# Performance work log

Measured on AMD Instinct MI355X. Metric: run time of the kernel, lower is better.

Reference implementation:

```python
import jax, jax.numpy as jnp
import numpy as np

EPS = 1e-5

def setup_inputs() -> dict:
    key = jax.random.key(0)
    ks = jax.random.split(key, 10)
    B, S, C, Q, D = 16, 2048, 768, 1024, 64
    clamp3_features = jax.random.normal(ks[0], (B, S, C), dtype=jnp.float32)
    residual = jax.random.normal(ks[1], (B, S, Q), dtype=jnp.float32)
    # params (xavier-ish scale; up-proj given small random values instead of zeros
    # so the output is non-trivial for correctness testing)
    Wproj = jax.random.normal(ks[2], (Q, C), dtype=jnp.float32) * (1.0 / np.sqrt(C))
    Wdown = jax.random.normal(ks[3], (D, Q), dtype=jnp.float32) * (1.0 / np.sqrt(Q))
    gamma = jnp.ones((D,), dtype=jnp.float32)
    beta = jnp.zeros((D,), dtype=jnp.float32)
    Wl1 = jax.random.normal(ks[4], (D, D), dtype=jnp.float32) * (1.0 / np.sqrt(D))
    bl1 = jnp.zeros((D,), dtype=jnp.float32)
    Wl2 = jax.random.normal(ks[5], (D, D), dtype=jnp.float32) * (1.0 / np.sqrt(D))
    bl2 = jnp.zeros((D,), dtype=jnp.float32)
    Wup = jax.random.normal(ks[6], (Q, D), dtype=jnp.float32) * (1.0 / np.sqrt(D))
    return {"clamp3_features": clamp3_features, "residual": residual,
            "Wproj": Wproj, "Wdown": Wdown, "gamma": gamma, "beta": beta,
            "Wl1": Wl1, "bl1": bl1, "Wl2": Wl2, "bl2": bl2, "Wup": Wup}

def _layernorm(x, gamma, beta):
    mu = jnp.mean(x, axis=-1, keepdims=True)
    var = jnp.mean(jnp.square(x - mu), axis=-1, keepdims=True)
    return (x - mu) * jax.lax.rsqrt(var + EPS) * gamma + beta

def reference(clamp3_features, residual, Wproj, Wdown, gamma, beta, Wl1, bl1, Wl2, bl2, Wup):
    # projection (no bias) -> down (no bias) -> LayerNorm
    projected = jnp.einsum('bsc,qc->bsq', clamp3_features, Wproj)
    down = jnp.einsum('bsq,dq->bsd', projected, Wdown)
    normed = _layernorm(down, gamma, beta)
    # SwiGLU: swish(l1(x)) * l2(x)
    o1 = jnp.einsum('bsd,ed->bse', normed, Wl1) + bl1
    swish = o1 * jax.nn.sigmoid(o1)
    gate = jnp.einsum('bsd,ed->bse', normed, Wl2) + bl2
    activated = swish * gate  # dropout is identity in eval mode
    up = jnp.einsum('bsd,qd->bsq', activated, Wup)
    return residual + up
```

## Files before the change

### kernel.cpp

```cpp
#include <hip/hip_runtime.h>


#define CDIM 768
#define QDIM 1024

typedef __attribute__((ext_vector_type(8))) short bf16x8;
typedef __attribute__((ext_vector_type(4))) float f32x4;

__device__ __forceinline__ ushort f2bf(float f) {
  union { float f; unsigned u; } v; v.f = f;
  unsigned r = v.u + 0x7fffu + ((v.u >> 16) & 1u);
  return (ushort)(r >> 16);
}

__device__ __forceinline__ void gload16(const float* g, float* lds) {
  __builtin_amdgcn_global_load_lds(
      (const __attribute__((address_space(1))) void*)g,
      (__attribute__((address_space(3))) void*)lds, 16, 0, 0);
}

__global__ void k_wcomb(const float* __restrict__ Wproj, const float* __restrict__ Wdown,
                        float* __restrict__ part) {
  int bid = blockIdx.x;
  int cb = bid % 12, db = (bid / 12) % 8, qc = bid / 96;
  int l = threadIdx.x;
  int c = cb * 64 + l;
  float acc[8];
  #pragma unroll
  for (int i = 0; i < 8; ++i) acc[i] = 0.f;
  int q0 = qc * 128;
  for (int q = q0; q < q0 + 128; ++q) {
    float xp = Wproj[q * CDIM + c];
    #pragma unroll
    for (int i = 0; i < 8; ++i)
      acc[i] = fmaf(Wdown[(db * 8 + i) * QDIM + q], xp, acc[i]);
  }
  #pragma unroll
  for (int i = 0; i < 8; ++i)
    part[((size_t)qc * CDIM + c) * 64 + db * 8 + i] = acc[i];
}

__global__ void k_arrange(const float* __restrict__ part, const float* __restrict__ Wup,
                          const float* __restrict__ Wl1, const float* __restrict__ Wl2,
                          ushort* __restrict__ wcf, ushort* __restrict__ wupf,
                          ushort* __restrict__ wl1f, ushort* __restrict__ wl2f) {
  int idx = blockIdx.x * 256 + threadIdx.x;
  if (idx < 49152) {
    int i0 = idx;
    int j = i0 & 7, l = (i0 >> 3) & 63, t = i0 >> 9;
    int g = l >> 4, r16 = l & 15;
    int nf = t & 3, ks = t >> 2;
    int k = 32 * ks + 8 * g + j, n = 16 * nf + r16;
    float s = 0.f;
    #pragma unroll
    for (int qc = 0; qc < 8; ++qc) s += part[((size_t)qc * CDIM + k) * 64 + n];
    wcf[i0] = f2bf(s);
  } else if (idx < 49152 + 65536) {
    int i2 = idx - 49152;
    int j = i2 & 7, l = (i2 >> 3) & 63, t = i2 >> 9;
    int g = l >> 4, r16 = l & 15;
    int ks = t & 1, nf = t >> 1;
    int k = 32 * ks + 8 * g + j, n = 16 * nf + r16;
    wupf[i2] = f2bf(Wup[n * 64 + k]);
  } else if (idx < 49152 + 65536 + 4096) {
    int i3 = idx - (49152 + 65536);
    int j = i3 & 7, l = (i3 >> 3) & 63, t = i3 >> 9;
    int g = l >> 4, r16 = l & 15;
    int nf = t & 3, ks = t >> 2;
    int k = 32 * ks + 8 * g + j, e = 16 * nf + r16;
    wl1f[i3] = f2bf(Wl1[e * 64 + k]);
  } else {
    int i4 = idx - (49152 + 65536 + 4096);
    int j = i4 & 7, l = (i4 >> 3) & 63, t = i4 >> 9;
    int g = l >> 4, r16 = l & 15;
    int nf = t & 3, ks = t >> 2;
    int k = 32 * ks + 8 * g + j, e = 16 * nf + r16;
    wl2f[i4] = f2bf(Wl2[e * 64 + k]);
  }
}

__global__ __launch_bounds__(256, 6)
void k_act(const float* __restrict__ xg,
           const float* __restrict__ gamma, const float* __restrict__ beta,
           const float* __restrict__ bl1, const float* __restrict__ bl2,
           const ushort* __restrict__ wcf,
           const ushort* __restrict__ wl1f, const ushort* __restrict__ wl2f,
           ushort* __restrict__ ag) {
  __shared__ ushort smem[12416];
  ushort (*x_lds)[776] = reinterpret_cast<ushort(*)[776]>(smem);
  float  (*d_lds)[68]  = reinterpret_cast<float (*)[68]>(smem);
  ushort (*n_lds)[72]  = reinterpret_cast<ushort(*)[72]>(reinterpret_cast<char*>(smem) + 4608);

  const int tid = threadIdx.x;
  const int w = tid >> 6, l = tid & 63, g = l >> 4, r16 = l & 15;
  const int row0 = blockIdx.x * 16;

  #pragma unroll
  for (int i = 0; i < 12; ++i) {
    int f4 = i * 256 + tid;
    int r = f4 / 192;
    int c4 = (f4 - r * 192) * 4;
    const float4 v = *reinterpret_cast<const float4*>(xg + (size_t)(row0 + r) * CDIM + c4);
    ushort4 b;
    b.x = f2bf(v.x); b.y = f2bf(v.y); b.z = f2bf(v.z); b.w = f2bf(v.w);
    *reinterpret_cast<ushort4*>(&x_lds[r][c4]) = b;
  }
  __syncthreads();

  f32x4 dacc = {0.f, 0.f, 0.f, 0.f};
  #pragma unroll 8
  for (int ks = 0; ks < 24; ++ks) {
    bf16x8 a = *reinterpret_cast<const bf16x8*>(&x_lds[r16][ks * 32 + 8 * g]);
    bf16x8 b = *reinterpret_cast<const bf16x8*>(wcf + ((size_t)(ks * 4 + w) * 64 + l) * 8);
    dacc = __builtin_amdgcn_mfma_f32_16x16x32_bf16(a, b, dacc, 0, 0, 0);
  }
  __syncthreads();
  #pragma unroll
  for (int rg = 0; rg < 4; ++rg) d_lds[4 * g + rg][16 * w + r16] = dacc[rg];
  __syncthreads();

  {
    int row = 4 * w + g;
    f32x4 v = *reinterpret_cast<const f32x4*>(&d_lds[row][4 * r16]);
    float s  = v[0] + v[1] + v[2] + v[3];
    float sq = v[0]*v[0] + v[1]*v[1] + v[2]*v[2] + v[3]*v[3];
    #pragma unroll
    for (int m = 1; m < 16; m <<= 1) {
      s  += __shfl_xor(s, m, 64);
      sq += __shfl_xor(sq, m, 64);
    }
    float mu  = s * (1.f / 64.f);
    float var = sq * (1.f / 64.f) - mu * mu;
    float rs  = rsqrtf(var + 1e-5f);
    const float4 gm = *reinterpret_cast<const float4*>(gamma + 4 * r16);
    const float4 bt = *reinterpret_cast<const float4*>(beta  + 4 * r16);
    ushort4 nb;
    nb.x = f2bf((v[0] - mu) * rs * gm.x + bt.x);
    nb.y = f2bf((v[1] - mu) * rs * gm.y + bt.y);
    nb.z = f2bf((v[2] - mu) * rs * gm.z + bt.z);
    nb.w = f2bf((v[3] - mu) * rs * gm.w + bt.w);
    *reinterpret_cast<ushort4*>(&n_lds[row][4 * r16]) = nb;
  }
  __syncthreads();

  {
    bf16x8 a0 = *reinterpret_cast<const bf16x8*>(&n_lds[r16][8 * g]);
    bf16x8 a1 = *reinterpret_cast<const bf16x8*>(&n_lds[r16][32 + 8 * g]);
    bf16x8 b10 = *reinterpret_cast<const bf16x8*>(wl1f + ((size_t)(0 * 4 + w) * 64 + l) * 8);
    bf16x8 b11 = *reinterpret_cast<const bf16x8*>(wl1f + ((size_t)(1 * 4 + w) * 64 + l) * 8);
    bf16x8 b20 = *reinterpret_cast<const bf16x8*>(wl2f + ((size_t)(0 * 4 + w) * 64 + l) * 8);
    bf16x8 b21 = *reinterpret_cast<const bf16x8*>(wl2f + ((size_t)(1 * 4 + w) * 64 + l) * 8);
    f32x4 z = {0.f, 0.f, 0.f, 0.f};
    f32x4 acc1 = __builtin_amdgcn_mfma_f32_16x16x32_bf16(a0, b10, z, 0, 0, 0);
    acc1 = __builtin_amdgcn_mfma_f32_16x16x32_bf16(a1, b11, acc1, 0, 0, 0);
    f32x4 acc2 = __builtin_amdgcn_mfma_f32_16x16x32_bf16(a0, b20, z, 0, 0, 0);
    acc2 = __builtin_amdgcn_mfma_f32_16x16x32_bf16(a1, b21, acc2, 0, 0, 0);
    float bv1 = bl1[16 * w + r16];
    float bv2 = bl2[16 * w + r16];
    #pragma unroll
    for (int rg = 0; rg < 4; ++rg) {
      float o1 = acc1[rg] + bv1;
      float o2 = acc2[rg] + bv2;
      float sw = o1 / (1.f + __expf(-o1));
      ag[(size_t)(row0 + 4 * g + rg) * 64 + 16 * w + r16] = f2bf(sw * o2);
    }
  }
}

__global__ __launch_bounds__(256, 2)
void k_up(const ushort* __restrict__ ag, const float* __restrict__ resg,
          const ushort* __restrict__ wupf, float* __restrict__ outg) {
  __shared__ float res_lds[4][16][256];
  const int tid = threadIdx.x;
  const int w = tid >> 6, l = tid & 63, g = l >> 4, r16 = l & 15;
  const int row0 = blockIdx.x * 16;

  const bf16x8 af0 = *reinterpret_cast<const bf16x8*>(ag + (size_t)(row0 + r16) * 64 + 8 * g);
  const bf16x8 af1 = *reinterpret_cast<const bf16x8*>(ag + (size_t)(row0 + r16) * 64 + 32 + 8 * g);

  f32x4 acc[16];
  #pragma unroll
  for (int nfl = 0; nfl < 16; ++nfl) {
    int nf = 16 * w + nfl;
    bf16x8 b0 = *reinterpret_cast<const bf16x8*>(wupf + ((size_t)(nf * 2 + 0) * 64 + l) * 8);
    bf16x8 b1 = *reinterpret_cast<const bf16x8*>(wupf + ((size_t)(nf * 2 + 1) * 64 + l) * 8);
    f32x4 t = {0.f, 0.f, 0.f, 0.f};
    t = __builtin_amdgcn_mfma_f32_16x16x32_bf16(b0, af0, t, 0, 0, 0);
    acc[nfl] = __builtin_amdgcn_mfma_f32_16x16x32_bf16(b1, af1, t, 0, 0, 0);
  }
  __builtin_amdgcn_sched_barrier(0);

  #pragma unroll
  for (int i = 0; i < 16; ++i) {
    const float* gsrc = resg + (size_t)(row0 + i) * QDIM + 256 * w + 4 * ((l + i) & 63);
    gload16(gsrc, &res_lds[w][i][0]);
  }
  asm volatile("s_waitcnt vmcnt(0)" ::: "memory");
  __builtin_amdgcn_sched_barrier(0);

  #pragma unroll
  for (int nfl = 0; nfl < 16; ++nfl) {
    int qr = (4 * nfl + g - r16) & 63;
    const f32x4 rv = *reinterpret_cast<const f32x4*>(&res_lds[w][r16][4 * qr]);
    f32x4 o = rv + acc[nfl];
    f32x4* dst = reinterpret_cast<f32x4*>(
        outg + (size_t)(row0 + r16) * QDIM + 16 * (16 * w + nfl) + 4 * g);
    __builtin_nontemporal_store(o, dst);
  }
}

extern "C" void kernel_launch(void* const* d_in, const int* in_sizes, int n_in,
                              void* d_out, int out_size, void* d_ws, size_t ws_size,
                              hipStream_t stream) {
  (void)in_sizes; (void)n_in; (void)out_size; (void)ws_size;
  const float* x     = (const float*)d_in[0];
  const float* resid = (const float*)d_in[1];
  const float* Wproj = (const float*)d_in[2];
  const float* Wdown = (const float*)d_in[3];
  const float* gamma = (const float*)d_in[4];
  const float* beta  = (const float*)d_in[5];
  const float* Wl1   = (const float*)d_in[6];
  const float* bl1   = (const float*)d_in[7];
  const float* Wl2   = (const float*)d_in[8];
  const float* bl2   = (const float*)d_in[9];
  const float* Wup   = (const float*)d_in[10];
  float* out = (float*)d_out;

  char* ws = (char*)d_ws;
  float*  part = (float*)(ws);
  ushort* wcf  = (ushort*)(ws + 1572864);
  ushort* wupf = (ushort*)(ws + 1671168);
  ushort* wl1f = (ushort*)(ws + 1802240);
  ushort* wl2f = (ushort*)(ws + 1810432);
  ushort* ag   = (ushort*)(ws + 1818624);

  k_wcomb  <<<768, 64, 0, stream>>>(Wproj, Wdown, part);
  k_arrange<<<480, 256, 0, stream>>>(part, Wup, Wl1, Wl2, wcf, wupf, wl1f, wl2f);
  k_act    <<<2048, 256, 0, stream>>>(x, gamma, beta, bl1, bl2, wcf, wl1f, wl2f, ag);
  k_up     <<<2048, 256, 0, stream>>>(ag, resid, wupf, out);
}
```

Measured before the change: 103.7 us.

## Make k_up persistent over row tiles with double-buffered residual prefetch

Rewrites k_up so each 512-thread block handles 128 rows in eight 16-row tiles. The Wup fragments stay in registers across tiles, and the next tile's activations and residual are prefetched into a double-buffered, XOR-swizzled LDS region while the current tile runs MFMA. The goal is to overlap residual loads with compute and stop reloading weights for every block. The costs are fewer blocks (one per CU), hand-tuned vmcnt waits that depend on compiler load ordering, and plain stores in place of nontemporal ones.

```diff
diff --git a/kernel.cpp b/kernel.cpp
--- a/kernel.cpp
+++ b/kernel.cpp
@@ -167,45 +167,77 @@
   }
 }
 
-__global__ __launch_bounds__(256, 2)
+__global__ __launch_bounds__(512, 1)
 void k_up(const ushort* __restrict__ ag, const float* __restrict__ resg,
           const ushort* __restrict__ wupf, float* __restrict__ outg) {
-  __shared__ float res_lds[4][16][256];
+  __shared__ float res_lds[2][8][16][128];
   const int tid = threadIdx.x;
   const int w = tid >> 6, l = tid & 63, g = l >> 4, r16 = l & 15;
-  const int row0 = blockIdx.x * 16;
-
-  const bf16x8 af0 = *reinterpret_cast<const bf16x8*>(ag + (size_t)(row0 + r16) * 64 + 8 * g);
-  const bf16x8 af1 = *reinterpret_cast<const bf16x8*>(ag + (size_t)(row0 + r16) * 64 + 32 + 8 * g);
-
-  f32x4 acc[16];
-  #pragma unroll
-  for (int nfl = 0; nfl < 16; ++nfl) {
-    int nf = 16 * w + nfl;
-    bf16x8 b0 = *reinterpret_cast<const bf16x8*>(wupf + ((size_t)(nf * 2 + 0) * 64 + l) * 8);
-    bf16x8 b1 = *reinterpret_cast<const bf16x8*>(wupf + ((size_t)(nf * 2 + 1) * 64 + l) * 8);
-    f32x4 t = {0.f, 0.f, 0.f, 0.f};
-    t = __builtin_amdgcn_mfma_f32_16x16x32_bf16(b0, af0, t, 0, 0, 0);
-    acc[nfl] = __builtin_amdgcn_mfma_f32_16x16x32_bf16(b1, af1, t, 0, 0, 0);
-  }
-  __builtin_amdgcn_sched_barrier(0);
-
-  #pragma unroll
-  for (int i = 0; i < 16; ++i) {
-    const float* gsrc = resg + (size_t)(row0 + i) * QDIM + 256 * w + 4 * ((l + i) & 63);
-    gload16(gsrc, &res_lds[w][i][0]);
-  }
-  asm volatile("s_waitcnt vmcnt(0)" ::: "memory");
-  __builtin_amdgcn_sched_barrier(0);
-
-  #pragma unroll
-  for (int nfl = 0; nfl < 16; ++nfl) {
-    int qr = (4 * nfl + g - r16) & 63;
-    const f32x4 rv = *reinterpret_cast<const f32x4*>(&res_lds[w][r16][4 * qr]);
-    f32x4 o = rv + acc[nfl];
-    f32x4* dst = reinterpret_cast<f32x4*>(
-        outg + (size_t)(row0 + r16) * QDIM + 16 * (16 * w + nfl) + 4 * g);
-    __builtin_nontemporal_store(o, dst);
+  const int blk_row0 = blockIdx.x * 128;
+
+  bf16x8 wf[16];
+  #pragma unroll
+  for (int nfl = 0; nfl < 8; ++nfl) {
+    size_t nf = 8 * w + nfl;
+    wf[2 * nfl + 0] = *reinterpret_cast<const bf16x8*>(wupf + ((nf * 2 + 0) * 64 + l) * 8);
+    wf[2 * nfl + 1] = *reinterpret_cast<const bf16x8*>(wupf + ((nf * 2 + 1) * 64 + l) * 8);
+  }
+
+  bf16x8 af0[2], af1[2];
+
+  {
+    const int trow0 = blk_row0;
+    af0[0] = *reinterpret_cast<const bf16x8*>(ag + (size_t)(trow0 + r16) * 64 + 8 * g);
+    af1[0] = *reinterpret_cast<const bf16x8*>(ag + (size_t)(trow0 + r16) * 64 + 32 + 8 * g);
+    float* base = &res_lds[0][w][0][0];
+    #pragma unroll
+    for (int i = 0; i < 8; ++i) {
+      const int r = 2 * i + (l >> 5);
+      const int sp = (l & 31) ^ (r & 7);
+      gload16(resg + (size_t)(trow0 + r) * QDIM + 128 * w + 4 * sp, base + i * 256);
+    }
+  }
+
+  #pragma unroll
+  for (int t = 0; t < 8; ++t) {
+    const int nt = (t + 1) & 7;
+    const int nb = (t + 1) & 1;
+    const int cb = t & 1;
+
+    __builtin_amdgcn_sched_barrier(0);
+    {
+      const int trow0 = blk_row0 + nt * 16;
+      af0[nb] = *reinterpret_cast<const bf16x8*>(ag + (size_t)(trow0 + r16) * 64 + 8 * g);
+      af1[nb] = *reinterpret_cast<const bf16x8*>(ag + (size_t)(trow0 + r16) * 64 + 32 + 8 * g);
+      float* base = &res_lds[nb][w][0][0];
+      #pragma unroll
+      for (int i = 0; i < 8; ++i) {
+        const int r = 2 * i + (l >> 5);
+        const int sp = (l & 31) ^ (r & 7);
+        gload16(resg + (size_t)(trow0 + r) * QDIM + 128 * w + 4 * sp, base + i * 256);
+      }
+    }
+    __builtin_amdgcn_sched_barrier(0);
+    if (t == 0) { asm volatile("s_waitcnt vmcnt(10)" ::: "memory"); }
+    else        { asm volatile("s_waitcnt vmcnt(18)" ::: "memory"); }
+    __builtin_amdgcn_sched_barrier(0);
+
+    const int trow0 = blk_row0 + t * 16;
+    f32x4 acc[8];
+    #pragma unroll
+    for (int nfl = 0; nfl < 8; ++nfl) {
+      f32x4 z = {0.f, 0.f, 0.f, 0.f};
+      z = __builtin_amdgcn_mfma_f32_16x16x32_bf16(wf[2 * nfl + 0], af0[cb], z, 0, 0, 0);
+      acc[nfl] = __builtin_amdgcn_mfma_f32_16x16x32_bf16(wf[2 * nfl + 1], af1[cb], z, 0, 0, 0);
+    }
+    #pragma unroll
+    for (int nfl = 0; nfl < 8; ++nfl) {
+      const int sp = (4 * nfl + g) ^ (r16 & 7);
+      const f32x4 rv = *reinterpret_cast<const f32x4*>(&res_lds[cb][w][r16][4 * sp]);
+      f32x4 o = rv + acc[nfl];
+      *reinterpret_cast<f32x4*>(
+          outg + (size_t)(trow0 + r16) * QDIM + 128 * w + 16 * nfl + 4 * g) = o;
+    }
   }
 }
 
@@ -237,5 +269,5 @@
   k_wcomb  <<<768, 64, 0, stream>>>(Wproj, Wdown, part);
   k_arrange<<<480, 256, 0, stream>>>(part, Wup, Wl1, Wl2, wcf, wupf, wl1f, wl2f);
   k_act    <<<2048, 256, 0, stream>>>(x, gamma, beta, bl1, bl2, wcf, wl1f, wl2f, ag);
-  k_up     <<<2048, 256, 0, stream>>>(ag, resid, wupf, out);
-}
+  k_up     <<<256, 512, 0, stream>>>(ag, resid, wupf, out);
+}
```

After: 132.4 us. 1.28x slower.
